# Kernel tuning notes

Measured on AMD Instinct MI355X. Metric: run time of the kernel, lower is better.

## Reference

```python
import jax, jax.numpy as jnp
import numpy as np
from jax import lax

E = 3  # num_experts

def _maxpool2(x):
    return lax.reduce_window(x, -jnp.inf, lax.max, (1, 1, 2, 2), (1, 1, 2, 2), 'VALID')

def _mixed_conv(x, experts, routing, stride, pad):
    # per-sample expert-mixed convolution via grouped conv trick
    B, Ci, H, W = x.shape
    _, Co, _, k, _ = experts.shape
    kern = jnp.einsum('be,eoikl->boikl', routing, experts).reshape(B * Co, Ci, k, k)
    y = lax.conv_general_dilated(
        x.reshape(1, B * Ci, H, W), kern, (stride, stride),
        [(pad, pad), (pad, pad)],
        dimension_numbers=('NCHW', 'OIHW', 'NCHW'),
        feature_group_count=B)
    return y.reshape(B, Co, y.shape[2], y.shape[3])

def _dyres_conv(x, experts, rw, rb, stride=1, pad=1):
    # DyRes mode 'A': routing from avg-pool + spatial-std descriptors, softmax over experts
    avg = x.mean((2, 3))
    std = x.std((2, 3))
    r = jax.nn.softmax((avg + std) @ rw.T + rb, axis=-1)  # [B, E]
    return _mixed_conv(x, experts, r, stride, pad)

def _cond_conv(x, experts, rw, rb, stride=1, pad=1):
    # CondConv: sigmoid routing from global average pool
    r = jax.nn.sigmoid(x.mean((2, 3)) @ rw.T + rb)  # [B, E]
    return _mixed_conv(x, experts, r, stride, pad)

def _conv_init(key, co, ci, k):
    return jax.random.normal(key, (E, co, ci, k, k), jnp.float32) * np.sqrt(2.0 / (ci * k * k)).astype(np.float32)

def setup_inputs() -> dict:
    key = jax.random.key(0)
    ks = jax.random.split(key, 20)
    B = 512
    d = {}
    d['x'] = jax.random.normal(ks[0], (B, 3, 32, 32), jnp.float32)
    d['dw1'] = _conv_init(ks[1], 64, 3, 3)
    d['rw1'] = jax.random.normal(ks[2], (E, 3), jnp.float32) * 0.1
    d['rb1'] = jnp.zeros((E,), jnp.float32)
    d['dw2'] = _conv_init(ks[3], 192, 64, 3)
    d['rw2'] = jax.random.normal(ks[4], (E, 64), jnp.float32) * 0.1
    d['rb2'] = jnp.zeros((E,), jnp.float32)
    d['dw3'] = _conv_init(ks[5], 384, 192, 3)
    d['rw3'] = jax.random.normal(ks[6], (E, 192), jnp.float32) * 0.1
    d['rb3'] = jnp.zeros((E,), jnp.float32)
    d['cw4'] = _conv_init(ks[7], 256, 384, 3)
    d['cr4w'] = jax.random.normal(ks[8], (E, 384), jnp.float32) * 0.1
    d['cr4b'] = jnp.zeros((E,), jnp.float32)
    d['cw5'] = _conv_init(ks[9], 256, 256, 3)
    d['cr5w'] = jax.random.normal(ks[10], (E, 256), jnp.float32) * 0.1
    d['cr5b'] = jnp.zeros((E,), jnp.float32)
    d['fw1'] = jax.random.normal(ks[11], (4096, 1024), jnp.float32) * np.sqrt(2.0 / 1024).astype(np.float32)
    d['fb1'] = jnp.zeros((4096,), jnp.float32)
    d['fw2'] = jax.random.normal(ks[12], (4096, 4096), jnp.float32) * np.sqrt(2.0 / 4096).astype(np.float32)
    d['fb2'] = jnp.zeros((4096,), jnp.float32)
    d['fw3'] = jax.random.normal(ks[13], (100, 4096), jnp.float32) * np.sqrt(1.0 / 4096).astype(np.float32)
    d['fb3'] = jnp.zeros((100,), jnp.float32)
    return d

def reference(x, dw1, rw1, rb1, dw2, rw2, rb2, dw3, rw3, rb3,
              cw4, cr4w, cr4b, cw5, cr5w, cr5b,
              fw1, fb1, fw2, fb2, fw3, fb3):
    h = jax.nn.relu(_dyres_conv(x, dw1, rw1, rb1, stride=2))   # [B,64,16,16]
    h = _maxpool2(h)                                           # [B,64,8,8]
    h = jax.nn.relu(_dyres_conv(h, dw2, rw2, rb2))             # [B,192,8,8]
    h = _maxpool2(h)                                           # [B,192,4,4]
    h = jax.nn.relu(_dyres_conv(h, dw3, rw3, rb3))             # [B,384,4,4]
    h = jax.nn.relu(_cond_conv(h, cw4, cr4w, cr4b))            # [B,256,4,4]
    h = jax.nn.relu(_cond_conv(h, cw5, cr5w, cr5b))            # [B,256,4,4]
    h = _maxpool2(h)                                           # [B,256,2,2]
    h = h.reshape(h.shape[0], -1)                              # [B,1024]
    h = jax.nn.relu(h @ fw1.T + fb1)
    h = jax.nn.relu(h @ fw2.T + fb2)
    return h @ fw3.T + fb3                                     # [B,100]
```

## Files before the change

kernel.cpp:

```cpp
#include <hip/hip_runtime.h>
#include <math.h>


typedef unsigned short u16;
typedef unsigned int u32;
typedef short bf16x8 __attribute__((ext_vector_type(8)));
typedef float f32x4 __attribute__((ext_vector_type(4)));

__device__ __forceinline__ u16 bf16_rne(float f) {
    u32 u = __float_as_uint(f);
    return (u16)((u + 0x7fffu + ((u >> 16) & 1u)) >> 16);
}
__device__ __forceinline__ u32 packsplit(float v) {
    u16 h = bf16_rne(v);
    float hf = __uint_as_float((u32)h << 16);
    u16 l = bf16_rne(v - hf);
    return ((u32)h << 16) | l;
}
__device__ __forceinline__ float unpackf(u32 p) {
    return __uint_as_float(p & 0xffff0000u) + __uint_as_float(p << 16);
}
__device__ __forceinline__ int xcd_swz(int bid, int n) {
    if ((n & 7) != 0) return bid;
    int cpx = n >> 3;
    return (bid & 7) * cpx + (bid >> 3);
}

__global__ __launch_bounds__(256)
void wsplit_kernel(const float* __restrict__ W, u16* __restrict__ whi,
                   u16* __restrict__ wlo, int total, int Kper, int Kpad)
{
    int idx = blockIdx.x * 256 + threadIdx.x;
    if (idx >= total) return;
    int r = idx / Kpad, k = idx - r * Kpad;
    float v = (k < Kper) ? W[(size_t)r * Kper + k] : 0.f;
    u16 h = bf16_rne(v);
    whi[idx] = h;
    wlo[idx] = bf16_rne(v - __uint_as_float((u32)h << 16));
}

__global__ __launch_bounds__(256)
void wsplit_cl_kernel(const float* __restrict__ W, u16* __restrict__ whi,
                      u16* __restrict__ wlo, int total, int Ci)
{
    int idx = blockIdx.x * 256 + threadIdx.x;
    if (idx >= total) return;
    int Kper = 9 * Ci;
    int r = idx / Kper, kp = idx - r * Kper;
    int cell = kp / Ci, ci = kp - cell * Ci;
    float v = W[(size_t)r * Kper + ci * 9 + cell];
    u16 h = bf16_rne(v);
    whi[idx] = h;
    wlo[idx] = bf16_rne(v - __uint_as_float((u32)h << 16));
}

__global__ __launch_bounds__(64)
void stats_kernel(const float* __restrict__ actv, float* __restrict__ s,
                  int C, int HW, int use_std)
{
    int idx = blockIdx.x;
    size_t base = (size_t)idx * HW;
    int lane = threadIdx.x;
    float sum = 0.f, sq = 0.f;
    const float* p = actv + base;
    for (int i = lane; i < HW; i += 64) { float v = p[i]; sum += v; sq += v * v; }
#pragma unroll
    for (int off = 32; off > 0; off >>= 1) {
        sum += __shfl_down(sum, off);
        sq  += __shfl_down(sq, off);
    }
    if (lane == 0) {
        float inv = 1.f / (float)HW;
        float mean = sum * inv;
        float var = sq * inv - mean * mean;
        float outv = mean;
        if (use_std) outv += sqrtf(fmaxf(var, 0.f));
        s[idx] = outv;
    }
}

__global__ __launch_bounds__(384)
void stats_cl_kernel(const u32* __restrict__ act, float* __restrict__ s,
                     int H2, int W2, int C, int use_std)
{
    int b = blockIdx.x, c = threadIdx.x;
    int Hin = H2 - 2, Win = W2 - 2;
    float sum = 0.f, sq = 0.f;
    for (int h = 0; h < Hin; ++h)
        for (int w = 0; w < Win; ++w) {
            float v = unpackf(act[(((size_t)b * H2 + h + 1) * W2 + w + 1) * C + c]);
            sum += v; sq += v * v;
        }
    float inv = 1.f / (float)(Hin * Win);
    float mean = sum * inv;
    float var = sq * inv - mean * mean;
    float outv = mean;
    if (use_std) outv += sqrtf(fmaxf(var, 0.f));
    s[b * C + c] = outv;
}

__global__ __launch_bounds__(64)
void routing_kernel(const float* __restrict__ s, const float* __restrict__ rw,
                    const float* __restrict__ rb, float* __restrict__ r,
                    int C, int softmax_mode)
{
    int b = blockIdx.x;
    int lane = threadIdx.x;
    float d0 = 0.f, d1 = 0.f, d2 = 0.f;
    for (int c = lane; c < C; c += 64) {
        float sv = s[b * C + c];
        d0 += sv * rw[c];
        d1 += sv * rw[C + c];
        d2 += sv * rw[2 * C + c];
    }
#pragma unroll
    for (int off = 32; off > 0; off >>= 1) {
        d0 += __shfl_down(d0, off);
        d1 += __shfl_down(d1, off);
        d2 += __shfl_down(d2, off);
    }
    if (lane == 0) {
        d0 += rb[0]; d1 += rb[1]; d2 += rb[2];
        if (softmax_mode) {
            float mx = fmaxf(d0, fmaxf(d1, d2));
            float e0 = expf(d0 - mx), e1 = expf(d1 - mx), e2 = expf(d2 - mx);
            float inv = 1.f / (e0 + e1 + e2);
            r[b * 3 + 0] = e0 * inv;
            r[b * 3 + 1] = e1 * inv;
            r[b * 3 + 2] = e2 * inv;
        } else {
            r[b * 3 + 0] = 1.f / (1.f + expf(-d0));
            r[b * 3 + 1] = 1.f / (1.f + expf(-d1));
            r[b * 3 + 2] = 1.f / (1.f + expf(-d2));
        }
    }
}

template<int CI, int H2, int W2, int LGS, int LGOW>
__global__ __launch_bounds__(256, 2)
void cgemm_cl_kernel(const u16* __restrict__ Whi, const u16* __restrict__ Wlo,
                     const u32* __restrict__ Bpk, const float* __restrict__ rptr,
                     float* __restrict__ Cout, int M, int N, int Kper, int Kchunk)
{
    __shared__ __align__(16) u16 Bh[2][128 * 40], Bl[2][128 * 40];
    const int tid = threadIdx.x;
    const int bx = xcd_swz(blockIdx.x, gridDim.x);
    const int n0 = bx << 7, m0 = blockIdx.y << 7;
    const int kq0 = blockIdx.z * Kchunk;

    const int nB = tid & 127, kOff = (tid >> 7) << 4;

    const int nn = n0 + nB;
    const int bB = nn >> LGS;
    const int sidx = nn & ((1 << LGS) - 1);
    const int oh = sidx >> LGOW, ow = sidx & ((1 << LGOW) - 1);
    const long nBase = ((long)(bB * H2 + oh) * W2 + ow) * CI;

    const int lane = tid & 63, wv = tid >> 6;
    const int lm = lane & 15, qd = lane >> 4;
    const int wm = (wv & 1) << 6, wn = (wv >> 1) << 6;

    float rsv[3][4];
#pragma unroll
    for (int ni = 0; ni < 4; ++ni) {
        int n = n0 + wn + ni * 16 + lm;
        int b = n >> LGS;
#pragma unroll
        for (int e = 0; e < 3; ++e) rsv[e][ni] = rptr[b * 3 + e];
    }

    f32x4 acc[4][4], accS[4][4];
#pragma unroll
    for (int i = 0; i < 4; ++i)
#pragma unroll
        for (int j = 0; j < 4; ++j) {
            acc[i][j]  = (f32x4){0.f, 0.f, 0.f, 0.f};
            accS[i][j] = (f32x4){0.f, 0.f, 0.f, 0.f};
        }

    const int nkz = Kchunk >> 5;
    const int NS = 3 * nkz;

    int kL = kq0;
    uint4 pQ0, pQ1, pQ2, pQ3;
    int eA = 0, kA = kq0;
    bf16x8 aH[4], aL[4];
    const size_t aRowOff = ((size_t)(m0 + wm + lm)) * Kper + qd * 8;
    const size_t aMiStep = (size_t)16 * Kper;
    const size_t aEStep  = (size_t)M * Kper;

    auto LOAD_B = [&]() {
        int k = kL + kOff;
        int cell = k / CI;
        int ci0 = k - cell * CI;
        int kh = (cell * 11) >> 5;
        int kw = cell - kh * 3;
        const u32* bp = Bpk + (nBase + (long)((kh * W2 + kw) * CI + ci0));
        pQ0 = *(const uint4*)bp;
        pQ1 = *(const uint4*)(bp + 4);
        pQ2 = *(const uint4*)(bp + 8);
        pQ3 = *(const uint4*)(bp + 12);
        kL += 32; if (kL == kq0 + Kchunk) kL = kq0;
    };
    auto LOAD_A = [&]() {
        const u16* hp = Whi + (size_t)eA * aEStep + aRowOff + kA;
        const u16* lp = Wlo + (size_t)eA * aEStep + aRowOff + kA;
#pragma unroll
        for (int mi = 0; mi < 4; ++mi) {
            aH[mi] = *(const bf16x8*)(hp + (size_t)mi * aMiStep);
            aL[mi] = *(const bf16x8*)(lp + (size_t)mi * aMiStep);
        }
        kA += 32; if (kA == kq0 + Kchunk) { kA = kq0; ++eA; }
    };
    auto STORE_B = [&](int buf) {
        u32 qv[16] = {pQ0.x, pQ0.y, pQ0.z, pQ0.w, pQ1.x, pQ1.y, pQ1.z, pQ1.w,
                      pQ2.x, pQ2.y, pQ2.z, pQ2.w, pQ3.x, pQ3.y, pQ3.z, pQ3.w};
        u32 hw[8], lw[8];
#pragma unroll
        for (int j = 0; j < 8; ++j) {
            u32 p0 = qv[2 * j], p1 = qv[2 * j + 1];
            hw[j] = (p0 >> 16) | (p1 & 0xffff0000u);
            lw[j] = (p0 & 0xffffu) | (p1 << 16);
        }
        *(uint4*)(&Bh[buf][nB * 40 + kOff])     = make_uint4(hw[0], hw[1], hw[2], hw[3]);
        *(uint4*)(&Bh[buf][nB * 40 + kOff + 8]) = make_uint4(hw[4], hw[5], hw[6], hw[7]);
        *(uint4*)(&Bl[buf][nB * 40 + kOff])     = make_uint4(lw[0], lw[1], lw[2], lw[3]);
        *(uint4*)(&Bl[buf][nB * 40 + kOff + 8]) = make_uint4(lw[4], lw[5], lw[6], lw[7]);
    };
    auto COMPUTE = [&](int buf) {
        __builtin_amdgcn_s_setprio(1);
#pragma unroll
        for (int ni = 0; ni < 4; ++ni) {
            int row = wn + ni * 16 + lm;
            bf16x8 bh = *(const bf16x8*)(&Bh[buf][row * 40 + qd * 8]);
            bf16x8 bl = *(const bf16x8*)(&Bl[buf][row * 40 + qd * 8]);
#pragma unroll
            for (int mi = 0; mi < 4; ++mi) {
                f32x4 c = acc[mi][ni];
                c = __builtin_amdgcn_mfma_f32_16x16x32_bf16(aL[mi], bh, c, 0, 0, 0);
                c = __builtin_amdgcn_mfma_f32_16x16x32_bf16(aH[mi], bl, c, 0, 0, 0);
                c = __builtin_amdgcn_mfma_f32_16x16x32_bf16(aH[mi], bh, c, 0, 0, 0);
                acc[mi][ni] = c;
            }
        }
        __builtin_amdgcn_s_setprio(0);
    };

    LOAD_B();
    LOAD_A();
    int s = 0, buf = 0;
#pragma unroll
    for (int e = 0; e < 3; ++e) {
        for (int t = 0; t < nkz; ++t) {
            STORE_B(buf);
            if (s + 1 < NS) LOAD_B();
            asm volatile("s_waitcnt lgkmcnt(0)\n\ts_barrier" ::: "memory");
            COMPUTE(buf);
            if (s + 1 < NS) LOAD_A();
            buf ^= 1; ++s;
        }
#pragma unroll
        for (int mi = 0; mi < 4; ++mi)
#pragma unroll
            for (int ni = 0; ni < 4; ++ni) {
                accS[mi][ni] += acc[mi][ni] * rsv[e][ni];
                acc[mi][ni] = (f32x4){0.f, 0.f, 0.f, 0.f};
            }
    }

    const bool atom = (gridDim.z > 1);
#pragma unroll
    for (int ni = 0; ni < 4; ++ni) {
        int n = n0 + wn + ni * 16 + lm;
#pragma unroll
        for (int mi = 0; mi < 4; ++mi)
#pragma unroll
            for (int r = 0; r < 4; ++r) {
                int m = m0 + wm + mi * 16 + qd * 4 + r;
                if (m >= M) continue;
                float v = accS[mi][ni][r];
                if (atom) atomicAdd(&Cout[(size_t)n * M + m], v);
                else      Cout[(size_t)n * M + m] = v;
            }
    }
}

__global__ __launch_bounds__(256, 2)
void cgemm_l1_kernel(const u16* __restrict__ Whi, const u16* __restrict__ Wlo,
                     const u32* __restrict__ Bpk, const float* __restrict__ rptr,
                     float* __restrict__ Cout, int M, int N)
{
    __shared__ __align__(16) u16 Ah[2][128 * 40], Al[2][128 * 40];
    __shared__ __align__(16) u16 Bh[2][128 * 40], Bl[2][128 * 40];
    const int tid = threadIdx.x;
    const int bx = xcd_swz(blockIdx.x, gridDim.x);
    const int n0 = bx << 7;
    const int Kper = 27, Kpad = 32;
    const int H = 32, W = 32;

    const int rowA = tid >> 1, kh16 = (tid & 1) << 4;
    const int nB = tid & 127, kOff = (tid >> 7) << 4;

    const int nn = n0 + nB;
    const int bB = nn >> 8;
    const int sidx = nn & 255;
    const int ohs = (sidx >> 4) * 2 - 1;
    const int ows = (sidx & 15) * 2 - 1;
    const long nBase = (long)bB * 3072 + (long)ohs * W + ows;

    const int lane = tid & 63, wv = tid >> 6;
    const int lm = lane & 15, qd = lane >> 4;
    const int wm = (wv & 1) << 6, wn = (wv >> 1) << 6;

    float rsv[3][4];
#pragma unroll
    for (int ni = 0; ni < 4; ++ni) {
        int n = n0 + wn + ni * 16 + lm;
        int b = n >> 8;
#pragma unroll
        for (int e = 0; e < 3; ++e) rsv[e][ni] = rptr[b * 3 + e];
    }

    f32x4 acc[4][4], accS[4][4];
#pragma unroll
    for (int i = 0; i < 4; ++i)
#pragma unroll
        for (int j = 0; j < 4; ++j) {
            acc[i][j]  = (f32x4){0.f, 0.f, 0.f, 0.f};
            accS[i][j] = (f32x4){0.f, 0.f, 0.f, 0.f};
        }

    const int mg = rowA;
    int eL = 0;
    uint4 pA0, pA1, pA2, pA3;
    u32 pB[16];

    auto LOAD = [&]() {
        size_t aOff = ((size_t)(eL * M + mg)) * Kpad + kh16;
        const u16* hp = Whi + aOff;
        const u16* lp = Wlo + aOff;
        pA0 = *(const uint4*)hp; pA1 = *(const uint4*)(hp + 8);
        pA2 = *(const uint4*)lp; pA3 = *(const uint4*)(lp + 8);
#pragma unroll
        for (int j = 0; j < 16; ++j) {
            int k = kOff + j;
            int ci = (int)((unsigned)k / 9u);
            int r9 = k - ci * 9;
            int kh = (int)(((unsigned)r9 * 11u) >> 5);
            int kw = r9 - kh * 3;
            int ih = ohs + kh, iw = ows + kw;
            u32 p = 0;
            if (k < Kper && (unsigned)ih < (unsigned)H && (unsigned)iw < (unsigned)W)
                p = Bpk[nBase + (long)ci * 1024 + kh * W + kw];
            pB[j] = p;
        }
    };
    auto STORE = [&](int buf) {
        *(uint4*)(&Ah[buf][rowA * 40 + kh16])     = pA0;
        *(uint4*)(&Ah[buf][rowA * 40 + kh16 + 8]) = pA1;
        *(uint4*)(&Al[buf][rowA * 40 + kh16])     = pA2;
        *(uint4*)(&Al[buf][rowA * 40 + kh16 + 8]) = pA3;
        u32 hw[8], lw[8];
#pragma unroll
        for (int j = 0; j < 8; ++j) {
            u32 p0 = pB[2 * j], p1 = pB[2 * j + 1];
            hw[j] = (p0 >> 16) | (p1 & 0xffff0000u);
            lw[j] = (p0 & 0xffffu) | (p1 << 16);
        }
        *(uint4*)(&Bh[buf][nB * 40 + kOff])     = make_uint4(hw[0], hw[1], hw[2], hw[3]);
        *(uint4*)(&Bh[buf][nB * 40 + kOff + 8]) = make_uint4(hw[4], hw[5], hw[6], hw[7]);
        *(uint4*)(&Bl[buf][nB * 40 + kOff])     = make_uint4(lw[0], lw[1], lw[2], lw[3]);
        *(uint4*)(&Bl[buf][nB * 40 + kOff + 8]) = make_uint4(lw[4], lw[5], lw[6], lw[7]);
    };
    auto COMPUTE = [&](int buf) {
        bf16x8 ah[4], al[4];
#pragma unroll
        for (int mi = 0; mi < 4; ++mi) {
            int row = wm + mi * 16 + lm;
            ah[mi] = *(const bf16x8*)(&Ah[buf][row * 40 + qd * 8]);
            al[mi] = *(const bf16x8*)(&Al[buf][row * 40 + qd * 8]);
        }
        __builtin_amdgcn_s_setprio(1);
#pragma unroll
        for (int ni = 0; ni < 4; ++ni) {
            int row = wn + ni * 16 + lm;
            bf16x8 bh = *(const bf16x8*)(&Bh[buf][row * 40 + qd * 8]);
            bf16x8 bl = *(const bf16x8*)(&Bl[buf][row * 40 + qd * 8]);
#pragma unroll
            for (int mi = 0; mi < 4; ++mi) {
                f32x4 c = acc[mi][ni];
                c = __builtin_amdgcn_mfma_f32_16x16x32_bf16(al[mi], bh, c, 0, 0, 0);
                c = __builtin_amdgcn_mfma_f32_16x16x32_bf16(ah[mi], bl, c, 0, 0, 0);
                c = __builtin_amdgcn_mfma_f32_16x16x32_bf16(ah[mi], bh, c, 0, 0, 0);
                acc[mi][ni] = c;
            }
        }
        __builtin_amdgcn_s_setprio(0);
    };

    LOAD(); ++eL;
    int buf = 0;
#pragma unroll
    for (int e = 0; e < 3; ++e) {
        STORE(buf);
        if (e < 2) { LOAD(); ++eL; }
        asm volatile("s_waitcnt lgkmcnt(0)\n\ts_barrier" ::: "memory");
        COMPUTE(buf);
        buf ^= 1;
#pragma unroll
        for (int mi = 0; mi < 4; ++mi)
#pragma unroll
            for (int ni = 0; ni < 4; ++ni) {
                accS[mi][ni] += acc[mi][ni] * rsv[e][ni];
                acc[mi][ni] = (f32x4){0.f, 0.f, 0.f, 0.f};
            }
    }

#pragma unroll
    for (int ni = 0; ni < 4; ++ni) {
        int n = n0 + wn + ni * 16 + lm;
#pragma unroll
        for (int mi = 0; mi < 4; ++mi)
#pragma unroll
            for (int r = 0; r < 4; ++r) {
                int m = wm + mi * 16 + qd * 4 + r;
                if (m >= M) continue;
                Cout[(size_t)n * M + m] = accS[mi][ni][r];
            }
    }
}

template<int BIAS, int TROUT>
__global__ __launch_bounds__(256)
void mgemm_kernel(const u16* __restrict__ Whi, const u16* __restrict__ Wlo,
                  const u32* __restrict__ Bpk, const float* __restrict__ bias,
                  float* __restrict__ Cout,
                  int M, int N, int Kpad, int Kchunk)
{
    __shared__ __align__(16) u16 Ah[128 * 40], Al[128 * 40];
    __shared__ __align__(16) u32 Bp[128 * 36];
    const int tid = threadIdx.x;
    const int n0 = blockIdx.x << 7, m0 = blockIdx.y << 7;
    const int bz = blockIdx.z;
    const int kq0 = bz * Kchunk;

    const int rowA = tid >> 1, kh16 = (tid & 1) << 4;
    const int nB = tid & 127, kOff = (tid >> 7) << 4;

    const int lane = tid & 63, wv = tid >> 6;
    const int lm = lane & 15, qd = lane >> 4;
    const int wm = (wv & 1) << 6, wn = (wv >> 1) << 6;

    f32x4 acc[4][4];
#pragma unroll
    for (int i = 0; i < 4; ++i)
#pragma unroll
        for (int j = 0; j < 4; ++j)
            acc[i][j] = (f32x4){0.f, 0.f, 0.f, 0.f};

    for (int kq = kq0; kq < kq0 + Kchunk; kq += 32) {
        {
            int mg = m0 + rowA;
            uint4 h0 = {0,0,0,0}, h1 = {0,0,0,0}, l0 = {0,0,0,0}, l1 = {0,0,0,0};
            if (mg < M) {
                const u16* hp = Whi + (size_t)mg * Kpad + kq + kh16;
                const u16* lp = Wlo + (size_t)mg * Kpad + kq + kh16;
                h0 = *(const uint4*)hp; h1 = *(const uint4*)(hp + 8);
                l0 = *(const uint4*)lp; l1 = *(const uint4*)(lp + 8);
            }
            *(uint4*)(&Ah[rowA * 40 + kh16])     = h0;
            *(uint4*)(&Ah[rowA * 40 + kh16 + 8]) = h1;
            *(uint4*)(&Al[rowA * 40 + kh16])     = l0;
            *(uint4*)(&Al[rowA * 40 + kh16 + 8]) = l1;
        }
        {
            const u32* bp = Bpk + (size_t)(n0 + nB) * Kpad + kq + kOff;
            uint4 q0 = *(const uint4*)bp;
            uint4 q1 = *(const uint4*)(bp + 4);
            uint4 q2 = *(const uint4*)(bp + 8);
            uint4 q3 = *(const uint4*)(bp + 12);
            *(uint4*)(&Bp[nB * 36 + kOff])      = q0;
            *(uint4*)(&Bp[nB * 36 + kOff + 4])  = q1;
            *(uint4*)(&Bp[nB * 36 + kOff + 8])  = q2;
            *(uint4*)(&Bp[nB * 36 + kOff + 12]) = q3;
        }
        __syncthreads();
        {
            bf16x8 ah[4], al[4];
#pragma unroll
            for (int mi = 0; mi < 4; ++mi) {
                int row = wm + mi * 16 + lm;
                ah[mi] = *(const bf16x8*)(&Ah[row * 40 + qd * 8]);
                al[mi] = *(const bf16x8*)(&Al[row * 40 + qd * 8]);
            }
#pragma unroll
            for (int ni = 0; ni < 4; ++ni) {
                int row = wn + ni * 16 + lm;
                const u32* bp = &Bp[row * 36 + qd * 8];
                uint4 p0 = *(const uint4*)bp;
                uint4 p1 = *(const uint4*)(bp + 4);
                union { u32 w[4]; bf16x8 v; } bh, bl;
                bh.w[0] = (p0.x >> 16) | (p0.y & 0xffff0000u);
                bl.w[0] = (p0.x & 0xffffu) | (p0.y << 16);
                bh.w[1] = (p0.z >> 16) | (p0.w & 0xffff0000u);
                bl.w[1] = (p0.z & 0xffffu) | (p0.w << 16);
                bh.w[2] = (p1.x >> 16) | (p1.y & 0xffff0000u);
                bl.w[2] = (p1.x & 0xffffu) | (p1.y << 16);
                bh.w[3] = (p1.z >> 16) | (p1.w & 0xffff0000u);
                bl.w[3] = (p1.z & 0xffffu) | (p1.w << 16);
#pragma unroll
                for (int mi = 0; mi < 4; ++mi) {
                    f32x4 c = acc[mi][ni];
                    c = __builtin_amdgcn_mfma_f32_16x16x32_bf16(al[mi], bh.v, c, 0, 0, 0);
                    c = __builtin_amdgcn_mfma_f32_16x16x32_bf16(ah[mi], bl.v, c, 0, 0, 0);
                    c = __builtin_amdgcn_mfma_f32_16x16x32_bf16(ah[mi], bh.v, c, 0, 0, 0);
                    acc[mi][ni] = c;
                }
            }
        }
        __syncthreads();
    }

#pragma unroll
    for (int ni = 0; ni < 4; ++ni) {
        int n = n0 + wn + ni * 16 + lm;
        if (n >= N) continue;
#pragma unroll
        for (int mi = 0; mi < 4; ++mi)
#pragma unroll
            for (int r = 0; r < 4; ++r) {
                int m = m0 + wm + mi * 16 + qd * 4 + r;
                if (m >= M) continue;
                float v = acc[mi][ni][r];
                if (BIAS && bz == 0) v += bias[m];
                if (TROUT) atomicAdd(&Cout[(size_t)n * M + m], v);
                else       atomicAdd(&Cout[(size_t)m * N + n], v);
            }
    }
}

__global__ __launch_bounds__(256)
void pack_kernel(const float* __restrict__ in, u32* __restrict__ outp, int count)
{
    int i = blockIdx.x * 256 + threadIdx.x;
    if (i >= count) return;
    outp[i] = packsplit(in[i]);
}

__global__ __launch_bounds__(256)
void pool_pack_cl_kernel(const float* __restrict__ in, u32* __restrict__ outp,
                         int Bn, int Hin, int Win, int C)
{
    int OH = Hin >> 1, OW = Win >> 1, H2 = OH + 2, W2 = OW + 2;
    int total = Bn * H2 * W2 * C;
    int i = blockIdx.x * 256 + threadIdx.x;
    if (i >= total) return;
    int c = i % C; int t = i / C;
    int w = t % W2; t /= W2;
    int h = t % H2; int b = t / H2;
    u32 pv = 0;
    if (h >= 1 && h <= OH && w >= 1 && w <= OW) {
        int oh = h - 1, ow = w - 1;
        const float* p = in + (((size_t)b * Hin + 2 * oh) * Win + 2 * ow) * C + c;
        size_t rs = (size_t)Win * C;
        float v = fmaxf(fmaxf(p[0], p[C]), fmaxf(p[rs], p[rs + C]));
        pv = packsplit(fmaxf(v, 0.f));
    }
    outp[i] = pv;
}

__global__ __launch_bounds__(256)
void pack_cl_kernel(const float* __restrict__ in, u32* __restrict__ outp,
                    int Bn, int Hin, int Win, int C)
{
    int H2 = Hin + 2, W2 = Win + 2;
    int total = Bn * H2 * W2 * C;
    int i = blockIdx.x * 256 + threadIdx.x;
    if (i >= total) return;
    int c = i % C; int t = i / C;
    int w = t % W2; t /= W2;
    int h = t % H2; int b = t / H2;
    u32 pv = 0;
    if (h >= 1 && h <= Hin && w >= 1 && w <= Win) {
        float v = in[(((size_t)b * Hin + (h - 1)) * Win + (w - 1)) * C + c];
        pv = packsplit(fmaxf(v, 0.f));
    }
    outp[i] = pv;
}

__global__ __launch_bounds__(256)
void pool_flatten_cl_kernel(const float* __restrict__ in, u32* __restrict__ outp)
{
    int i = blockIdx.x * 256 + threadIdx.x;
    if (i >= 512 * 1024) return;
    int b = i >> 10;
    int f = i & 1023;
    int c = f >> 2, sp = f & 3;
    int oh = sp >> 1, ow = sp & 1;
    const float* p = in + (((size_t)b * 4 + 2 * oh) * 4 + 2 * ow) * 256 + c;
    float v = fmaxf(fmaxf(p[0], p[256]), fmaxf(p[1024], p[1024 + 256]));
    outp[i] = packsplit(fmaxf(v, 0.f));
}

__global__ __launch_bounds__(256)
void tp_pack_kernel(const float* __restrict__ in, u32* __restrict__ outp,
                    int Mt, int Nt)
{
    __shared__ float t[32][33];
    int tx = threadIdx.x & 31, ty = threadIdx.x >> 5;
    int mB = blockIdx.x << 5, nB = blockIdx.y << 5;
#pragma unroll
    for (int i = 0; i < 4; ++i) {
        int mm = ty + i * 8;
        t[mm][tx] = in[(size_t)(mB + mm) * Nt + nB + tx];
    }
    __syncthreads();
#pragma unroll
    for (int i = 0; i < 4; ++i) {
        int nn = ty + i * 8;
        float v = fmaxf(t[tx][nn], 0.f);
        outp[(size_t)(nB + nn) * Mt + mB + tx] = packsplit(v);
    }
}

extern "C" void kernel_launch(void* const* d_in, const int* in_sizes, int n_in,
                              void* d_out, int out_size, void* d_ws, size_t ws_size,
                              hipStream_t stream)
{
    const float* x    = (const float*)d_in[0];
    const float* dw1  = (const float*)d_in[1];
    const float* rw1  = (const float*)d_in[2];
    const float* rb1  = (const float*)d_in[3];
    const float* dw2  = (const float*)d_in[4];
    const float* rw2  = (const float*)d_in[5];
    const float* rb2  = (const float*)d_in[6];
    const float* dw3  = (const float*)d_in[7];
    const float* rw3  = (const float*)d_in[8];
    const float* rb3  = (const float*)d_in[9];
    const float* cw4  = (const float*)d_in[10];
    const float* cr4w = (const float*)d_in[11];
    const float* cr4b = (const float*)d_in[12];
    const float* cw5  = (const float*)d_in[13];
    const float* cr5w = (const float*)d_in[14];
    const float* cr5b = (const float*)d_in[15];
    const float* fw1  = (const float*)d_in[16];
    const float* fb1  = (const float*)d_in[17];
    const float* fw2  = (const float*)d_in[18];
    const float* fb2  = (const float*)d_in[19];
    const float* fw3  = (const float*)d_in[20];
    const float* fb3  = (const float*)d_in[21];
    float* out = (float*)d_out;

    float* ws    = (float*)d_ws;
    float* r1    = ws;
    float* r2    = r1 + 1536;
    float* r3    = r2 + 1536;
    float* r4    = r3 + 1536;
    float* r5    = r4 + 1536;
    float* sdesc = ws + 8192 + 65536;
    const size_t REGION = 18874368;
    float* region = sdesc + 196608;
    float* slab   = region;
    u32*   a3u    = (u32*)(region + 4194304);
    u16*   regEnd = (u16*)(region + REGION);
    u32*   P1     = (u32*)(region + REGION);

    u16 *w1h = regEnd - 2*(size_t)6144,     *w1l = regEnd - (size_t)6144;
    u16 *w2h = regEnd - 2*(size_t)331776,   *w2l = regEnd - (size_t)331776;
    u16 *w3h = regEnd - 2*(size_t)1990656,  *w3l = regEnd - (size_t)1990656;
    u16 *w4h = regEnd - 2*(size_t)2654208,  *w4l = regEnd - (size_t)2654208;
    u16 *w5h = regEnd - 2*(size_t)1769472,  *w5l = regEnd - (size_t)1769472;
    u16 *f1h = regEnd - 2*(size_t)4194304,  *f1l = regEnd - (size_t)4194304;
    u16 *f2h = regEnd - 2*(size_t)16777216, *f2l = regEnd - (size_t)16777216;
    u16 *f3h = regEnd - 2*(size_t)409600,   *f3l = regEnd - (size_t)409600;

    u32* xpk   = P1;
    u32* a1    = P1;
    u32* a2    = P1;
    u32* a4    = P1;
    u32* hTpk  = P1;
    u32* f1pkT = P1 + 1048576;
    u32* f2pkT = P1 + 3145728;

    const int B = 512;

    pack_kernel<<<6144, 256, 0, stream>>>(x, xpk, 1572864);

    wsplit_kernel<<<24, 256, 0, stream>>>(dw1, w1h, w1l, 6144, 27, 32);
    stats_kernel<<<B * 3, 64, 0, stream>>>(x, sdesc, 3, 1024, 1);
    routing_kernel<<<B, 64, 0, stream>>>(sdesc, rw1, rb1, r1, 3, 1);
    cgemm_l1_kernel<<<dim3(1024, 1, 1), 256, 0, stream>>>(
        w1h, w1l, xpk, r1, slab, 64, 131072);
    pool_pack_cl_kernel<<<12800, 256, 0, stream>>>(slab, a1, B, 16, 16, 64);

    wsplit_cl_kernel<<<1296, 256, 0, stream>>>(dw2, w2h, w2l, 331776, 64);
    stats_cl_kernel<<<B, 64, 0, stream>>>(a1, sdesc, 10, 10, 64, 1);
    routing_kernel<<<B, 64, 0, stream>>>(sdesc, rw2, rb2, r2, 64, 1);
    cgemm_cl_kernel<64, 10, 10, 6, 3><<<dim3(256, 2, 1), 256, 0, stream>>>(
        w2h, w2l, a1, r2, slab, 192, 32768, 576, 576);
    pool_pack_cl_kernel<<<13824, 256, 0, stream>>>(slab, a2, B, 8, 8, 192);

    wsplit_cl_kernel<<<7776, 256, 0, stream>>>(dw3, w3h, w3l, 1990656, 192);
    stats_cl_kernel<<<B, 192, 0, stream>>>(a2, sdesc, 6, 6, 192, 1);
    routing_kernel<<<B, 64, 0, stream>>>(sdesc, rw3, rb3, r3, 192, 1);
    hipMemsetAsync(slab, 0, (size_t)8192 * 384 * 4, stream);
    cgemm_cl_kernel<192, 6, 6, 4, 2><<<dim3(64, 3, 2), 256, 0, stream>>>(
        w3h, w3l, a2, r3, slab, 384, 8192, 1728, 864);
    pack_cl_kernel<<<27648, 256, 0, stream>>>(slab, a3u, B, 4, 4, 384);

    wsplit_cl_kernel<<<10368, 256, 0, stream>>>(cw4, w4h, w4l, 2654208, 384);
    stats_cl_kernel<<<B, 384, 0, stream>>>(a3u, sdesc, 6, 6, 384, 0);
    routing_kernel<<<B, 64, 0, stream>>>(sdesc, cr4w, cr4b, r4, 384, 0);
    hipMemsetAsync(slab, 0, (size_t)8192 * 256 * 4, stream);
    cgemm_cl_kernel<384, 6, 6, 4, 2><<<dim3(64, 2, 4), 256, 0, stream>>>(
        w4h, w4l, a3u, r4, slab, 256, 8192, 3456, 864);
    pack_cl_kernel<<<18432, 256, 0, stream>>>(slab, a4, B, 4, 4, 256);

    wsplit_cl_kernel<<<6912, 256, 0, stream>>>(cw5, w5h, w5l, 1769472, 256);
    stats_cl_kernel<<<B, 256, 0, stream>>>(a4, sdesc, 6, 6, 256, 0);
    routing_kernel<<<B, 64, 0, stream>>>(sdesc, cr5w, cr5b, r5, 256, 0);
    hipMemsetAsync(slab, 0, (size_t)8192 * 256 * 4, stream);
    cgemm_cl_kernel<256, 6, 6, 4, 2><<<dim3(64, 2, 4), 256, 0, stream>>>(
        w5h, w5l, a4, r5, slab, 256, 8192, 2304, 576);

    pool_flatten_cl_kernel<<<2048, 256, 0, stream>>>(slab, hTpk);

    wsplit_kernel<<<16384, 256, 0, stream>>>(fw1, f1h, f1l, 4194304, 1024, 1024);
    hipMemsetAsync(slab, 0, (size_t)4096 * 512 * 4, stream);
    mgemm_kernel<1, 0><<<dim3(4, 32, 8), 256, 0, stream>>>(
        f1h, f1l, hTpk, fb1, slab, 4096, 512, 1024, 128);
    tp_pack_kernel<<<dim3(128, 16), 256, 0, stream>>>(slab, f1pkT, 4096, 512);

    wsplit_kernel<<<65536, 256, 0, stream>>>(fw2, f2h, f2l, 16777216, 4096, 4096);
    hipMemsetAsync(slab, 0, (size_t)4096 * 512 * 4, stream);
    mgemm_kernel<1, 0><<<dim3(4, 32, 8), 256, 0, stream>>>(
        f2h, f2l, f1pkT, fb2, slab, 4096, 512, 4096, 512);
    tp_pack_kernel<<<dim3(128, 16), 256, 0, stream>>>(slab, f2pkT, 4096, 512);

    wsplit_kernel<<<1600, 256, 0, stream>>>(fw3, f3h, f3l, 409600, 4096, 4096);
    hipMemsetAsync(out, 0, (size_t)512 * 100 * 4, stream);
    mgemm_kernel<1, 1><<<dim3(4, 1, 32), 256, 0, stream>>>(
        f3h, f3l, f2pkT, fb3, out, 100, 512, 4096, 128);
}
```

Measured before the change: 1.714 ms.

## Restructure conv GEMM to 256x256 tiles with LDS direct loads and expert split

```diff
diff --git a/kernel.cpp b/kernel.cpp
--- a/kernel.cpp
+++ b/kernel.cpp
@@ -137,150 +137,140 @@
 }
 
 template<int CI, int H2, int W2, int LGS, int LGOW>
-__global__ __launch_bounds__(256, 2)
+__global__ __launch_bounds__(256, 1)
 void cgemm_cl_kernel(const u16* __restrict__ Whi, const u16* __restrict__ Wlo,
                      const u32* __restrict__ Bpk, const float* __restrict__ rptr,
-                     float* __restrict__ Cout, int M, int N, int Kper, int Kchunk)
-{
-    __shared__ __align__(16) u16 Bh[2][128 * 40], Bl[2][128 * 40];
+                     float* __restrict__ Cout, int M, int N, int Kper,
+                     int Kchunk, int kz)
+{
+    __shared__ __align__(16) u16 AhS[2][256 * 32];
+    __shared__ __align__(16) u16 AlS[2][256 * 32];
+    __shared__ __align__(16) u32 BpS[2][256 * 32];
+
     const int tid = threadIdx.x;
+    const int lane = tid & 63, wv = tid >> 6;
     const int bx = xcd_swz(blockIdx.x, gridDim.x);
-    const int n0 = bx << 7, m0 = blockIdx.y << 7;
-    const int kq0 = blockIdx.z * Kchunk;
-
-    const int nB = tid & 127, kOff = (tid >> 7) << 4;
-
-    const int nn = n0 + nB;
-    const int bB = nn >> LGS;
-    const int sidx = nn & ((1 << LGS) - 1);
-    const int oh = sidx >> LGOW, ow = sidx & ((1 << LGOW) - 1);
-    const long nBase = ((long)(bB * H2 + oh) * W2 + ow) * CI;
-
-    const int lane = tid & 63, wv = tid >> 6;
+    const int n0 = bx << 8, m0 = blockIdx.y << 8;
+    const int bz = blockIdx.z;
+    const int eA = bz / kz;
+    const int kq0 = (bz - eA * kz) * Kchunk;
+
     const int lm = lane & 15, qd = lane >> 4;
-    const int wm = (wv & 1) << 6, wn = (wv >> 1) << 6;
-
-    float rsv[3][4];
-#pragma unroll
-    for (int ni = 0; ni < 4; ++ni) {
-        int n = n0 + wn + ni * 16 + lm;
-        int b = n >> LGS;
-#pragma unroll
-        for (int e = 0; e < 3; ++e) rsv[e][ni] = rptr[b * 3 + e];
-    }
-
-    f32x4 acc[4][4], accS[4][4];
-#pragma unroll
-    for (int i = 0; i < 4; ++i)
-#pragma unroll
-        for (int j = 0; j < 4; ++j) {
-            acc[i][j]  = (f32x4){0.f, 0.f, 0.f, 0.f};
-            accS[i][j] = (f32x4){0.f, 0.f, 0.f, 0.f};
-        }
-
-    const int nkz = Kchunk >> 5;
-    const int NS = 3 * nkz;
-
-    int kL = kq0;
-    uint4 pQ0, pQ1, pQ2, pQ3;
-    int eA = 0, kA = kq0;
-    bf16x8 aH[4], aL[4];
-    const size_t aRowOff = ((size_t)(m0 + wm + lm)) * Kper + qd * 8;
-    const size_t aMiStep = (size_t)16 * Kper;
-    const size_t aEStep  = (size_t)M * Kper;
-
-    auto LOAD_B = [&]() {
-        int k = kL + kOff;
-        int cell = k / CI;
-        int ci0 = k - cell * CI;
-        int kh = (cell * 11) >> 5;
-        int kw = cell - kh * 3;
-        const u32* bp = Bpk + (nBase + (long)((kh * W2 + kw) * CI + ci0));
-        pQ0 = *(const uint4*)bp;
-        pQ1 = *(const uint4*)(bp + 4);
-        pQ2 = *(const uint4*)(bp + 8);
-        pQ3 = *(const uint4*)(bp + 12);
-        kL += 32; if (kL == kq0 + Kchunk) kL = kq0;
+    const int wm = (wv & 1) << 7, wn = (wv >> 1) << 7;
+
+    u32 offs[16];
+    if (wv < 2) {
+#pragma unroll
+        for (int i = 0; i < 16; ++i) {
+            int row = i * 16 + (lane >> 2);
+            int slot = (lane & 3) ^ ((row >> 1) & 3);
+            offs[i] = (u32)((m0 + row) * Kper + slot * 8);
+        }
+    } else {
+        int rbase = (wv - 2) * 128;
+#pragma unroll
+        for (int i = 0; i < 16; ++i) {
+            int row = rbase + i * 8 + (lane >> 3);
+            int slot = (lane & 7) ^ (row & 7);
+            int n = n0 + row;
+            int bB = n >> LGS;
+            int sidx = n & ((1 << LGS) - 1);
+            int oh = sidx >> LGOW, ow = sidx & ((1 << LGOW) - 1);
+            offs[i] = (u32)(((bB * H2 + oh) * W2 + ow) * CI + slot * 4);
+        }
+    }
+
+    f32x4 acc[8][8];
+#pragma unroll
+    for (int i = 0; i < 8; ++i)
+#pragma unroll
+        for (int j = 0; j < 8; ++j)
+            acc[i][j] = (f32x4){0.f, 0.f, 0.f, 0.f};
+
+    const size_t aScalBase = (size_t)eA * M * Kper;
+
+    auto ISSUE = [&](int buf, int kI) {
+        if (wv < 2) {
+            const u16* gp = ((wv == 0) ? Whi : Wlo) + aScalBase + kI;
+            u16* lp = (wv == 0) ? &AhS[buf][0] : &AlS[buf][0];
+#pragma unroll
+            for (int i = 0; i < 16; ++i)
+                __builtin_amdgcn_global_load_lds(gp + offs[i], lp + i * 512, 16, 0, 0);
+        } else {
+            int cell = kI / CI;
+            int ci0 = kI - cell * CI;
+            int kh = (cell * 11) >> 5;
+            int kw = cell - kh * 3;
+            const u32* gp = Bpk + ((kh * W2 + kw) * CI + ci0);
+            u32* lp = &BpS[buf][(wv - 2) * 4096];
+#pragma unroll
+            for (int i = 0; i < 16; ++i)
+                __builtin_amdgcn_global_load_lds(gp + offs[i], lp + i * 256, 16, 0, 0);
+        }
     };
-    auto LOAD_A = [&]() {
-        const u16* hp = Whi + (size_t)eA * aEStep + aRowOff + kA;
-        const u16* lp = Wlo + (size_t)eA * aEStep + aRowOff + kA;
-#pragma unroll
-        for (int mi = 0; mi < 4; ++mi) {
-            aH[mi] = *(const bf16x8*)(hp + (size_t)mi * aMiStep);
-            aL[mi] = *(const bf16x8*)(lp + (size_t)mi * aMiStep);
-        }
-        kA += 32; if (kA == kq0 + Kchunk) { kA = kq0; ++eA; }
-    };
-    auto STORE_B = [&](int buf) {
-        u32 qv[16] = {pQ0.x, pQ0.y, pQ0.z, pQ0.w, pQ1.x, pQ1.y, pQ1.z, pQ1.w,
-                      pQ2.x, pQ2.y, pQ2.z, pQ2.w, pQ3.x, pQ3.y, pQ3.z, pQ3.w};
-        u32 hw[8], lw[8];
-#pragma unroll
-        for (int j = 0; j < 8; ++j) {
-            u32 p0 = qv[2 * j], p1 = qv[2 * j + 1];
-            hw[j] = (p0 >> 16) | (p1 & 0xffff0000u);
-            lw[j] = (p0 & 0xffffu) | (p1 << 16);
-        }
-        *(uint4*)(&Bh[buf][nB * 40 + kOff])     = make_uint4(hw[0], hw[1], hw[2], hw[3]);
-        *(uint4*)(&Bh[buf][nB * 40 + kOff + 8]) = make_uint4(hw[4], hw[5], hw[6], hw[7]);
-        *(uint4*)(&Bl[buf][nB * 40 + kOff])     = make_uint4(lw[0], lw[1], lw[2], lw[3]);
-        *(uint4*)(&Bl[buf][nB * 40 + kOff + 8]) = make_uint4(lw[4], lw[5], lw[6], lw[7]);
-    };
+
+    const int xm = (lm >> 1) & 3;
+
     auto COMPUTE = [&](int buf) {
+        bf16x8 ah[8], al[8];
+#pragma unroll
+        for (int mi = 0; mi < 8; ++mi) {
+            int row = wm + mi * 16 + lm;
+            int off = row * 32 + ((qd ^ xm) * 8);
+            ah[mi] = *(const bf16x8*)&AhS[buf][off];
+            al[mi] = *(const bf16x8*)&AlS[buf][off];
+        }
         __builtin_amdgcn_s_setprio(1);
 #pragma unroll
-        for (int ni = 0; ni < 4; ++ni) {
+        for (int ni = 0; ni < 8; ++ni) {
             int row = wn + ni * 16 + lm;
-            bf16x8 bh = *(const bf16x8*)(&Bh[buf][row * 40 + qd * 8]);
-            bf16x8 bl = *(const bf16x8*)(&Bl[buf][row * 40 + qd * 8]);
-#pragma unroll
-            for (int mi = 0; mi < 4; ++mi) {
+            int sw = row & 7;
+            const u32* bp = &BpS[buf][row * 32];
+            uint4 p0 = *(const uint4*)(bp + (((2 * qd) ^ sw) * 4));
+            uint4 p1 = *(const uint4*)(bp + (((2 * qd + 1) ^ sw) * 4));
+            union { u32 w[4]; bf16x8 v; } bh, bl;
+            bh.w[0] = (p0.x >> 16) | (p0.y & 0xffff0000u);
+            bl.w[0] = (p0.x & 0xffffu) | (p0.y << 16);
+            bh.w[1] = (p0.z >> 16) | (p0.w & 0xffff0000u);
+            bl.w[1] = (p0.z & 0xffffu) | (p0.w << 16);
+            bh.w[2] = (p1.x >> 16) | (p1.y & 0xffff0000u);
+            bl.w[2] = (p1.x & 0xffffu) | (p1.y << 16);
+            bh.w[3] = (p1.z >> 16) | (p1.w & 0xffff0000u);
+            bl.w[3] = (p1.z & 0xffffu) | (p1.w << 16);
+#pragma unroll
+            for (int mi = 0; mi < 8; ++mi) {
                 f32x4 c = acc[mi][ni];
-                c = __builtin_amdgcn_mfma_f32_16x16x32_bf16(aL[mi], bh, c, 0, 0, 0);
-                c = __builtin_amdgcn_mfma_f32_16x16x32_bf16(aH[mi], bl, c, 0, 0, 0);
-                c = __builtin_amdgcn_mfma_f32_16x16x32_bf16(aH[mi], bh, c, 0, 0, 0);
+                c = __builtin_amdgcn_mfma_f32_16x16x32_bf16(al[mi], bh.v, c, 0, 0, 0);
+                c = __builtin_amdgcn_mfma_f32_16x16x32_bf16(ah[mi], bl.v, c, 0, 0, 0);
+                c = __builtin_amdgcn_mfma_f32_16x16x32_bf16(ah[mi], bh.v, c, 0, 0, 0);
                 acc[mi][ni] = c;
             }
         }
         __builtin_amdgcn_s_setprio(0);
     };
 
-    LOAD_B();
-    LOAD_A();
-    int s = 0, buf = 0;
-#pragma unroll
-    for (int e = 0; e < 3; ++e) {
-        for (int t = 0; t < nkz; ++t) {
-            STORE_B(buf);
-            if (s + 1 < NS) LOAD_B();
-            asm volatile("s_waitcnt lgkmcnt(0)\n\ts_barrier" ::: "memory");
-            COMPUTE(buf);
-            if (s + 1 < NS) LOAD_A();
-            buf ^= 1; ++s;
-        }
-#pragma unroll
-        for (int mi = 0; mi < 4; ++mi)
-#pragma unroll
-            for (int ni = 0; ni < 4; ++ni) {
-                accS[mi][ni] += acc[mi][ni] * rsv[e][ni];
-                acc[mi][ni] = (f32x4){0.f, 0.f, 0.f, 0.f};
-            }
-    }
-
-    const bool atom = (gridDim.z > 1);
-#pragma unroll
-    for (int ni = 0; ni < 4; ++ni) {
+    const int NS = Kchunk >> 5;
+    int kI = kq0;
+    ISSUE(0, kI); kI += 32;
+    int buf = 0;
+    for (int s = 0; s < NS; ++s) {
+        asm volatile("s_waitcnt vmcnt(0) lgkmcnt(0)\n\ts_barrier" ::: "memory");
+        if (s + 1 < NS) { ISSUE(buf ^ 1, kI); kI += 32; }
+        COMPUTE(buf);
+        buf ^= 1;
+    }
+
+#pragma unroll
+    for (int ni = 0; ni < 8; ++ni) {
         int n = n0 + wn + ni * 16 + lm;
-#pragma unroll
-        for (int mi = 0; mi < 4; ++mi)
+        float rs = rptr[(n >> LGS) * 3 + eA];
+#pragma unroll
+        for (int mi = 0; mi < 8; ++mi)
 #pragma unroll
             for (int r = 0; r < 4; ++r) {
                 int m = m0 + wm + mi * 16 + qd * 4 + r;
                 if (m >= M) continue;
-                float v = accS[mi][ni][r];
-                if (atom) atomicAdd(&Cout[(size_t)n * M + m], v);
-                else      Cout[(size_t)n * M + m] = v;
+                atomicAdd(&Cout[(size_t)n * M + m], acc[mi][ni][r] * rs);
             }
     }
 }
@@ -696,32 +686,33 @@
     wsplit_cl_kernel<<<1296, 256, 0, stream>>>(dw2, w2h, w2l, 331776, 64);
     stats_cl_kernel<<<B, 64, 0, stream>>>(a1, sdesc, 10, 10, 64, 1);
     routing_kernel<<<B, 64, 0, stream>>>(sdesc, rw2, rb2, r2, 64, 1);
-    cgemm_cl_kernel<64, 10, 10, 6, 3><<<dim3(256, 2, 1), 256, 0, stream>>>(
-        w2h, w2l, a1, r2, slab, 192, 32768, 576, 576);
+    hipMemsetAsync(slab, 0, (size_t)192 * 32768 * 4, stream);
+    cgemm_cl_kernel<64, 10, 10, 6, 3><<<dim3(128, 1, 6), 256, 0, stream>>>(
+        w2h, w2l, a1, r2, slab, 192, 32768, 576, 288, 2);
     pool_pack_cl_kernel<<<13824, 256, 0, stream>>>(slab, a2, B, 8, 8, 192);
 
     wsplit_cl_kernel<<<7776, 256, 0, stream>>>(dw3, w3h, w3l, 1990656, 192);
     stats_cl_kernel<<<B, 192, 0, stream>>>(a2, sdesc, 6, 6, 192, 1);
     routing_kernel<<<B, 64, 0, stream>>>(sdesc, rw3, rb3, r3, 192, 1);
     hipMemsetAsync(slab, 0, (size_t)8192 * 384 * 4, stream);
-    cgemm_cl_kernel<192, 6, 6, 4, 2><<<dim3(64, 3, 2), 256, 0, stream>>>(
-        w3h, w3l, a2, r3, slab, 384, 8192, 1728, 864);
+    cgemm_cl_kernel<192, 6, 6, 4, 2><<<dim3(32, 2, 6), 256, 0, stream>>>(
+        w3h, w3l, a2, r3, slab, 384, 8192, 1728, 864, 2);
     pack_cl_kernel<<<27648, 256, 0, stream>>>(slab, a3u, B, 4, 4, 384);
 
     wsplit_cl_kernel<<<10368, 256, 0, stream>>>(cw4, w4h, w4l, 2654208, 384);
     stats_cl_kernel<<<B, 384, 0, stream>>>(a3u, sdesc, 6, 6, 384, 0);
     routing_kernel<<<B, 64, 0, stream>>>(sdesc, cr4w, cr4b, r4, 384, 0);
     hipMemsetAsync(slab, 0, (size_t)8192 * 256 * 4, stream);
-    cgemm_cl_kernel<384, 6, 6, 4, 2><<<dim3(64, 2, 4), 256, 0, stream>>>(
-        w4h, w4l, a3u, r4, slab, 256, 8192, 3456, 864);
+    cgemm_cl_kernel<384, 6, 6, 4, 2><<<dim3(32, 1, 12), 256, 0, stream>>>(
+        w4h, w4l, a3u, r4, slab, 256, 8192, 3456, 864, 4);
     pack_cl_kernel<<<18432, 256, 0, stream>>>(slab, a4, B, 4, 4, 256);
 
     wsplit_cl_kernel<<<6912, 256, 0, stream>>>(cw5, w5h, w5l, 1769472, 256);
     stats_cl_kernel<<<B, 256, 0, stream>>>(a4, sdesc, 6, 6, 256, 0);
     routing_kernel<<<B, 64, 0, stream>>>(sdesc, cr5w, cr5b, r5, 256, 0);
     hipMemsetAsync(slab, 0, (size_t)8192 * 256 * 4, stream);
-    cgemm_cl_kernel<256, 6, 6, 4, 2><<<dim3(64, 2, 4), 256, 0, stream>>>(
-        w5h, w5l, a4, r5, slab, 256, 8192, 2304, 576);
+    cgemm_cl_kernel<256, 6, 6, 4, 2><<<dim3(32, 1, 12), 256, 0, stream>>>(
+        w5h, w5l, a4, r5, slab, 256, 8192, 2304, 576, 4);
 
     pool_flatten_cl_kernel<<<2048, 256, 0, stream>>>(slab, hTpk);
 
```

Result: slower. 2.636 ms (+53.8%).
